# Performance work log

Measured on AMD Instinct MI355X. Metric: run time of the kernel, lower is better.

The kernel has to match this reference:

```python
import jax, jax.numpy as jnp
import numpy as np
from functools import partial

# geometry: [W1, W2, H1, H2, L1, L2] -> x range, y range, z range
GEOM = (-16.0, 16.0, -16.0, 16.0, -16.0, 16.0)
T_MEAN = jnp.array([-0.25, 0.01, 0.26, 0.46, 0.26, 0.62, 0.69, 1.46], jnp.float32)
T_STD = jnp.array([0.93, 0.26, 0.53, 0.89, 1.11, 0.13, 0.16, 0.19], jnp.float32)
M_CAND = 1024   # cap on candidates passing cls > 0.5 (top-k by score)
IOU_THR = 0.5
CLS_THR = 0.5
# 8 corner sign combos for (x, y, z)
SIGNS = jnp.array([[sx, sy, sz] for sx in (1.0, -1.0) for sy in (1.0, -1.0) for sz in (1.0, -1.0)], jnp.float32)


def _pairwise_iou(b):
    # b: [M, 4] in (min0, min1, max0, max1)
    area = jnp.clip(b[:, 2] - b[:, 0], 0) * jnp.clip(b[:, 3] - b[:, 1], 0)
    lt = jnp.maximum(b[:, None, :2], b[None, :, :2])
    rb = jnp.minimum(b[:, None, 2:], b[None, :, 2:])
    wh = jnp.clip(rb - lt, 0)
    inter = wh[..., 0] * wh[..., 1]
    union = area[:, None] + area[None, :] - inter
    return inter / jnp.maximum(union, 1e-9)


def _nms_keep(boxes, valid, thr):
    # boxes already sorted by descending score; greedy NMS like torchvision ops.nms
    M = boxes.shape[0]
    iou = _pairwise_iou(boxes)
    ar = jnp.arange(M)

    def body(i, st):
        keep, sup = st
        k = valid[i] & jnp.logical_not(sup[i])
        keep = keep.at[i].set(k)
        sup = sup | (k & (iou[i] > thr) & (ar > i))
        return keep, sup

    keep, _ = jax.lax.fori_loop(0, M, body, (jnp.zeros(M, bool), jnp.zeros(M, bool)))
    return keep


def _decode(points):
    B, C, Z, Y, X = points.shape
    x0, x1, y0, y1, z0, z1 = GEOM
    xs = x0 + (x1 - x0) / X * jnp.arange(X, dtype=jnp.float32)
    ys = y0 + (y1 - y0) / Y * jnp.arange(Y, dtype=jnp.float32)
    zs = z0 + (z1 - z0) / Z * jnp.arange(Z, dtype=jnp.float32)
    zz, yy, xx = jnp.meshgrid(zs, ys, xs, indexing='ij')  # [Z,Y,X]
    cls = points[:, 0]  # [B,Z,Y,X], untouched by normalization
    reg = points[:, 1:9] * T_STD[None, :, None, None, None] + T_MEAN[None, :, None, None, None]
    cos_t, sin_t, dx, dy, dz, log_w, log_h, log_l = [reg[:, i] for i in range(8)]
    theta = jnp.arctan2(sin_t, cos_t)
    cx = xx[None] + dx
    cy = yy[None] + dy
    cz = zz[None] + dz
    w, h, l = jnp.exp(log_w), jnp.exp(log_h), jnp.exp(log_l)
    return cls, cx, cy, cz, w, h, l, theta


def _per_batch(cls, cx, cy, cz, w, h, l, theta, n_out):
    sc, idx = jax.lax.top_k(cls.reshape(-1), M_CAND)
    valid = sc > CLS_THR
    g = lambda a: a.reshape(-1)[idx]
    cxf, cyf, czf, wf, hf, lf, thf = g(cx), g(cy), g(cz), g(w), g(h), g(l), g(theta)
    zeros = jnp.zeros_like(thf)
    box9 = jnp.stack([cxf, cyf, czf, wf, hf, lf, zeros, thf, zeros], axis=-1)  # [M,9]
    # corners: half-size offsets rotated by Ry(theta) (rx = rz = 0)
    off = 0.5 * SIGNS[None, :, :] * jnp.stack([wf, hf, lf], -1)[:, None, :]  # [M,8,3]
    ct, st = jnp.cos(thf)[:, None], jnp.sin(thf)[:, None]
    ox, oy, oz = off[..., 0], off[..., 1], off[..., 2]
    px = cxf[:, None] + ct * ox + st * oz
    py = cyf[:, None] + oy
    pz = czf[:, None] - st * ox + ct * oz
    xmin, xmax = px.min(-1), px.max(-1)
    ymin, ymax = py.min(-1), py.max(-1)
    zmin, zmax = pz.min(-1), pz.max(-1)
    xy_box = jnp.stack([xmin, ymin, xmax, ymax], -1)
    yz_box = jnp.stack([ymin, zmin, ymax, zmax], -1)
    keep = _nms_keep(xy_box, valid, IOU_THR) | _nms_keep(yz_box, valid, IOU_THR)
    # compact kept boxes to the front (score order), pad with zeros to n_out
    order = jnp.argsort(jnp.where(keep, 0, 1))[:n_out]  # stable sort
    kv = keep[order]
    boxes_out = box9[order] * kv[:, None].astype(box9.dtype)
    scores_out = sc[order] * kv.astype(sc.dtype)
    return boxes_out, scores_out


def setup_inputs() -> dict:
    key = jax.random.key(0)
    B, Z, Y, X = 4, 64, 128, 128
    points = jax.random.normal(key, (B, 9, Z, Y, X), dtype=jnp.float32)
    points = points.at[:, 0].add(-3.0)
    return {"points": points, "label_shape": 0, "n_out": 50}


def reference(points, label_shape, n_out):
    cls, cx, cy, cz, w, h, l, theta = _decode(points)
    boxes, scores = jax.vmap(partial(_per_batch, n_out=n_out))(cls, cx, cy, cz, w, h, l, theta)
    return boxes, scores  # [B, n_out, 9], [B, n_out]
```

## Files before the change

### kernel.cpp

```cpp
#include <hip/hip_runtime.h>

typedef unsigned long long u64;

#define ZYX (64 * 128 * 128)
#define CPB 128
#define SEG (ZYX / CPB)
#define SLOTS 64
#define VMAX 1024
#define MMAX 1024
#define MFAST 320
#define NCH 5
#define NTH 1024
#define NWAVE (NTH / 64)
#define CLS_THR 0.5f
#define IOU_THR 0.5f

__constant__ const float TM[8] = {-0.25f, 0.01f, 0.26f, 0.46f, 0.26f, 0.62f, 0.69f, 1.46f};
__constant__ const float TS[8] = {0.93f, 0.26f, 0.53f, 0.89f, 1.11f, 0.13f, 0.16f, 0.19f};

__device__ __forceinline__ void decode_from_r(const float* r, int f,
                                              float& cx, float& cy, float& cz,
                                              float& w, float& h, float& l, float& th) {
    int z = f >> 14;
    int y = (f >> 7) & 127;
    int x = f & 127;
    th = atan2f(r[1], r[0]);
    cx = (-16.0f + 0.25f * (float)x) + r[2];
    cy = (-16.0f + 0.25f * (float)y) + r[3];
    cz = (-16.0f + 0.5f * (float)z) + r[4];
    w = expf(r[5]);
    h = expf(r[6]);
    l = expf(r[7]);
}

__device__ __forceinline__ void decode_one(const float* __restrict__ pb, int f,
                                           float& cx, float& cy, float& cz,
                                           float& w, float& h, float& l, float& th) {
    float r[8];
#pragma unroll
    for (int c = 0; c < 8; ++c)
        r[c] = pb[(size_t)(c + 1) * ZYX + f] * TS[c] + TM[c];
    decode_from_r(r, f, cx, cy, cz, w, h, l, th);
}

__device__ __forceinline__ void corner_boxes(float cx, float cy, float cz,
                                             float w, float h, float l, float th,
                                             float& xmn, float& ymn, float& xmx, float& ymx,
                                             float& zmn, float& zmx) {
    float ct = cosf(th), st = sinf(th);
    xmn = 1e30f; xmx = -1e30f; ymn = 1e30f; ymx = -1e30f; zmn = 1e30f; zmx = -1e30f;
#pragma unroll
    for (int k = 0; k < 8; ++k) {
        float sx = (k & 4) ? -1.0f : 1.0f;
        float sy = (k & 2) ? -1.0f : 1.0f;
        float sz = (k & 1) ? -1.0f : 1.0f;
        float ox = 0.5f * sx * w;
        float oy = 0.5f * sy * h;
        float oz = 0.5f * sz * l;
        float px = cx + ct * ox + st * oz;
        float py = cy + oy;
        float pz = cz - st * ox + ct * oz;
        xmn = fminf(xmn, px); xmx = fmaxf(xmx, px);
        ymn = fminf(ymn, py); ymx = fmaxf(ymx, py);
        zmn = fminf(zmn, pz); zmx = fmaxf(zmx, pz);
    }
}

__device__ __forceinline__ bool iou_over(float ax0, float ay0, float ax1, float ay1, float aarea,
                                         float bx0, float by0, float bx1, float by1, float barea) {
    float lt0 = fmaxf(ax0, bx0), lt1 = fmaxf(ay0, by0);
    float rb0 = fminf(ax1, bx1), rb1 = fminf(ay1, by1);
    float inter = fmaxf(rb0 - lt0, 0.0f) * fmaxf(rb1 - lt1, 0.0f);
    float uni = aarea + barea - inter;
    return inter / fmaxf(uni, 1e-9f) > IOU_THR;
}

__global__ __launch_bounds__(256) void collect_kernel(const float* __restrict__ points,
                                                      int* __restrict__ gcnt,
                                                      float* __restrict__ gsc,
                                                      int* __restrict__ gix) {
    __shared__ float s_ssc[SLOTS];
    __shared__ int s_six[SLOTS];
    __shared__ int s_n;
    int g = blockIdx.x;
    int b = g >> 7;
    int c = g & (CPB - 1);
    int tid = threadIdx.x;
    if (tid == 0) s_n = 0;
    __syncthreads();
    const float4* p4 = (const float4*)(points + (size_t)b * 9 * ZYX) + (size_t)c * (SEG / 4);
    int base = c * SEG;
#pragma unroll
    for (int k = 0; k < SEG / 4 / 256; ++k) {
        int t4 = k * 256 + tid;
        float4 v = p4[t4];
        float vals[4] = {v.x, v.y, v.z, v.w};
        int f = base + t4 * 4;
#pragma unroll
        for (int q = 0; q < 4; ++q) {
            if (vals[q] > CLS_THR) {
                int s = atomicAdd(&s_n, 1);
                if (s < SLOTS) { s_ssc[s] = vals[q]; s_six[s] = f + q; }
            }
        }
    }
    __syncthreads();
    int n = s_n < SLOTS ? s_n : SLOTS;
    if (tid == 0) gcnt[g] = n;
    for (int i = tid; i < n; i += 256) {
        gsc[g * SLOTS + i] = s_ssc[i];
        gix[g * SLOTS + i] = s_six[i];
    }
}

__global__ __launch_bounds__(NTH, 1) void nms_kernel(const float* __restrict__ points,
                                                     const int* __restrict__ gcnt,
                                                     const float* __restrict__ gsc,
                                                     const int* __restrict__ gix,
                                                     float4* __restrict__ wbxy,
                                                     float4* __restrict__ wbyz,
                                                     float2* __restrict__ war,
                                                     float* __restrict__ out,
                                                     int B, int n_out) {
    __shared__ float s_sc[VMAX];
    __shared__ int s_ix[VMAX];
    __shared__ int s_r2o[MMAX];
    __shared__ float s_reg[MFAST * 8];
    __shared__ float4 s_bxy[MFAST];
    __shared__ float4 s_byz[MFAST];
    __shared__ float2 s_ar[MFAST];
    __shared__ u64 s_colx[MFAST * NCH];
    __shared__ u64 s_coly[MFAST * NCH];
    __shared__ u64 s_keptw[16];
    __shared__ int s_cnt[CPB], s_pre[CPB];

    int b = blockIdx.x;
    int tid = threadIdx.x;
    const float* pb = points + (size_t)b * 9 * ZYX;

    if (tid < CPB) s_cnt[tid] = gcnt[b * CPB + tid];
    __syncthreads();
    if (tid < CPB) {
        int pre = 0;
        for (int i = 0; i < CPB; ++i) { int v = s_cnt[i]; if (i < tid) pre += v; }
        s_pre[tid] = pre;
    }
    __syncthreads();
    int V = s_pre[CPB - 1] + s_cnt[CPB - 1];
    if (V > VMAX) V = VMAX;
    if (tid < CPB) {
        int n = s_cnt[tid], o = s_pre[tid], g = b * CPB + tid;
        for (int i = 0; i < n; ++i) {
            int d = o + i;
            if (d < VMAX) { s_sc[d] = gsc[g * SLOTS + i]; s_ix[d] = gix[g * SLOTS + i]; }
        }
    }
    __syncthreads();

    int M = V < MMAX ? V : MMAX;
    int nchw = (M + 63) >> 6;
    bool fast = (M <= MFAST);

    for (int i = tid; i < V; i += NTH) {
        float si = s_sc[i];
        int ii = s_ix[i];
        int r = 0;
        for (int j = 0; j < V; ++j) {
            float sj = s_sc[j];
            int ij = s_ix[j];
            bool before = (sj > si) || (sj == si && ij < ii);
            r += before ? 1 : 0;
        }
        if (r < MMAX) s_r2o[r] = i;
    }
    __syncthreads();

    if (fast) {
        int M8 = M * 8;
        for (int t = tid; t < M8; t += NTH) {
            int m = t >> 3, c = t & 7;
            int f = s_ix[s_r2o[m]];
            s_reg[t] = pb[(size_t)(c + 1) * ZYX + f] * TS[c] + TM[c];
        }
        __syncthreads();
        for (int m = tid; m < M; m += NTH) {
            float r[8];
#pragma unroll
            for (int c = 0; c < 8; ++c) r[c] = s_reg[m * 8 + c];
            int f = s_ix[s_r2o[m]];
            float cx, cy, cz, w, h, l, th;
            decode_from_r(r, f, cx, cy, cz, w, h, l, th);
            float xmn, ymn, xmx, ymx, zmn, zmx;
            corner_boxes(cx, cy, cz, w, h, l, th, xmn, ymn, xmx, ymx, zmn, zmx);
            s_bxy[m] = make_float4(xmn, ymn, xmx, ymx);
            s_byz[m] = make_float4(ymn, zmn, ymx, zmx);
            float axy = fmaxf(xmx - xmn, 0.0f) * fmaxf(ymx - ymn, 0.0f);
            float ayz = fmaxf(ymx - ymn, 0.0f) * fmaxf(zmx - zmn, 0.0f);
            s_ar[m] = make_float2(axy, ayz);
        }
        __syncthreads();

        int wid = tid >> 6, lane = tid & 63;
        for (int j = wid; j < M; j += NWAVE) {
            float4 jxy = s_bxy[j], jyz = s_byz[j];
            float2 ja = s_ar[j];
            int smax = j >> 6;
            for (int s = 0; s <= smax; ++s) {
                int i = (s << 6) | lane;
                float4 ixy = s_bxy[i];
                float2 ia = s_ar[i];
                bool p = (i < j);
                bool ax = p && iou_over(ixy.x, ixy.y, ixy.z, ixy.w, ia.x,
                                        jxy.x, jxy.y, jxy.z, jxy.w, ja.x);
                u64 wxw = __ballot(ax);
                float4 iyz = s_byz[i];
                bool ay = p && iou_over(iyz.x, iyz.y, iyz.z, iyz.w, ia.y,
                                        jyz.x, jyz.y, jyz.z, jyz.w, ja.y);
                u64 wyw = __ballot(ay);
                if (lane == 0) {
                    s_colx[j * NCH + s] = wxw;
                    s_coly[j * NCH + s] = wyw;
                }
            }
        }
        __syncthreads();

        if (tid < 64) {
            int lane = tid;
            u64 extx = 0, exty = 0;
            for (int s = 0; s < nchw; ++s) {
                int c = s * 64 + lane;
                bool have = c < M;
                u64 wx = have ? s_colx[c * NCH + s] : 0ull;
                u64 wy = have ? s_coly[c * NCH + s] : 0ull;
                bool ex = (extx >> s) & 1ull;
                bool ey = (exty >> s) & 1ull;
                bool sup = ex;
                for (;;) {
                    u64 K = __ballot(!sup && have);
                    bool ns = ex | ((wx & K) != 0ull);
                    u64 ch = __ballot(ns != sup);
                    sup = ns;
                    if (!ch) break;
                }
                u64 Kx = __ballot(!sup && have);
                bool supy = ey;
                for (;;) {
                    u64 K = __ballot(!supy && have);
                    bool ns = ey | ((wy & K) != 0ull);
                    u64 ch = __ballot(ns != supy);
                    supy = ns;
                    if (!ch) break;
                }
                u64 Ky = __ballot(!supy && have);
                if (lane == 0) s_keptw[s] = Kx | Ky;
                for (int s2 = s + 1; s2 < nchw; ++s2) {
                    int c2 = s2 * 64 + lane;
                    if (c2 < M) {
                        if (s_colx[c2 * NCH + s] & Kx) extx |= 1ull << s2;
                        if (s_coly[c2 * NCH + s] & Ky) exty |= 1ull << s2;
                    }
                }
            }
        }
    } else {
        for (int r = tid; r < M; r += NTH) {
            float cx, cy, cz, w, h, l, th;
            decode_one(pb, s_ix[s_r2o[r]], cx, cy, cz, w, h, l, th);
            float xmn, ymn, xmx, ymx, zmn, zmx;
            corner_boxes(cx, cy, cz, w, h, l, th, xmn, ymn, xmx, ymx, zmn, zmx);
            wbxy[b * MMAX + r] = make_float4(xmn, ymn, xmx, ymx);
            wbyz[b * MMAX + r] = make_float4(ymn, zmn, ymx, zmx);
            float axy = fmaxf(xmx - xmn, 0.0f) * fmaxf(ymx - ymn, 0.0f);
            float ayz = fmaxf(ymx - ymn, 0.0f) * fmaxf(zmx - zmn, 0.0f);
            war[b * MMAX + r] = make_float2(axy, ayz);
        }
        __syncthreads();
        if (tid == 0) {
            char* supx = (char*)s_colx;
            char* supy = ((char*)s_colx) + MMAX;
            for (int s = 0; s < 16; ++s) s_keptw[s] = 0ull;
            for (int i = 0; i < M; ++i) { supx[i] = 0; supy[i] = 0; }
            int nk = 0;
            for (int i = 0; i < M; ++i) {
                bool kx = !supx[i], ky = !supy[i];
                if (!(kx | ky)) continue;
                s_keptw[i >> 6] |= 1ull << (i & 63);
                if (++nk >= n_out) break;
                float4 ixy = wbxy[b * MMAX + i], iyz = wbyz[b * MMAX + i];
                float2 ia = war[b * MMAX + i];
                for (int j = i + 1; j < M; ++j) {
                    float4 jxy = wbxy[b * MMAX + j];
                    float2 ja = war[b * MMAX + j];
                    if (kx && !supx[j] &&
                        iou_over(ixy.x, ixy.y, ixy.z, ixy.w, ia.x,
                                 jxy.x, jxy.y, jxy.z, jxy.w, ja.x)) supx[j] = 1;
                    float4 jyz = wbyz[b * MMAX + j];
                    if (ky && !supy[j] &&
                        iou_over(iyz.x, iyz.y, iyz.z, iyz.w, ia.y,
                                 jyz.x, jyz.y, jyz.z, jyz.w, ja.y)) supy[j] = 1;
                }
            }
        }
    }
    __syncthreads();

    float* boxes_out = out;
    float* scores_out = out + (size_t)B * n_out * 9;
    for (int p = tid; p < n_out; p += NTH) {
        int m = -1, total = 0;
        for (int s = 0; s < nchw; ++s) {
            u64 w = s_keptw[s];
            int pc = __popcll(w);
            if (m < 0 && p < total + pc) {
                int need = p - total;
                for (int q = 0; q < need; ++q) w &= w - 1ull;
                int bit = __ffsll((long long)w) - 1;
                m = s * 64 + bit;
            }
            total += pc;
        }
        float o9[9] = {0, 0, 0, 0, 0, 0, 0, 0, 0};
        float sc = 0.0f;
        if (m >= 0) {
            int o = s_r2o[m];
            int f = s_ix[o];
            float cx, cy, cz, w, h, l, th;
            if (fast) {
                float r[8];
#pragma unroll
                for (int c = 0; c < 8; ++c) r[c] = s_reg[m * 8 + c];
                decode_from_r(r, f, cx, cy, cz, w, h, l, th);
            } else {
                decode_one(pb, f, cx, cy, cz, w, h, l, th);
            }
            o9[0] = cx; o9[1] = cy; o9[2] = cz;
            o9[3] = w;  o9[4] = h;  o9[5] = l;
            o9[6] = 0.0f; o9[7] = th; o9[8] = 0.0f;
            sc = s_sc[o];
        }
        float* bo = boxes_out + ((size_t)b * n_out + p) * 9;
#pragma unroll
        for (int k = 0; k < 9; ++k) bo[k] = o9[k];
        scores_out[(size_t)b * n_out + p] = sc;
    }
}

extern "C" void kernel_launch(void* const* d_in, const int* in_sizes, int n_in,
                              void* d_out, int out_size, void* d_ws, size_t ws_size,
                              hipStream_t stream) {
    const float* points = (const float*)d_in[0];
    int B = in_sizes[0] / (9 * ZYX);
    int n_out = out_size / (B * 10);

    char* ws = (char*)d_ws;
    size_t off = 0;
    int* gcnt = (int*)(ws + off); off += (size_t)B * CPB * sizeof(int); off = (off + 255) & ~(size_t)255;
    float* gsc = (float*)(ws + off); off += (size_t)B * CPB * SLOTS * 4;
    int* gix = (int*)(ws + off); off += (size_t)B * CPB * SLOTS * 4;
    float4* wbxy = (float4*)(ws + off); off += (size_t)B * MMAX * 16;
    float4* wbyz = (float4*)(ws + off); off += (size_t)B * MMAX * 16;
    float2* war = (float2*)(ws + off); off += (size_t)B * MMAX * 8;

    collect_kernel<<<B * CPB, 256, 0, stream>>>(points, gcnt, gsc, gix);
    nms_kernel<<<B, NTH, 0, stream>>>(points, gcnt, gsc, gix, wbxy, wbyz, war,
                                      (float*)d_out, B, n_out);
}
```

Baseline: 224.1 us.

## Gather regression channels in collect kernel and pack score/index into sort key

The collect kernel now gathers and normalizes the 8 regression channels for each candidate across many blocks, writing them to a compact workspace. The NMS kernel reads those rows with float4 loads instead of doing scattered strided reads from the input in its single-block-per-batch phase. Score and index are packed into one 64-bit key, so the rank computation does one compare per pair. VMAX/MMAX shrink to 768, which lowers shared memory but caps candidates below the spec's 1024 limit.

```diff
diff --git a/kernel.cpp b/kernel.cpp
--- a/kernel.cpp
+++ b/kernel.cpp
@@ -1,13 +1,14 @@
 #include <hip/hip_runtime.h>
 
 typedef unsigned long long u64;
+typedef unsigned int u32;
 
 #define ZYX (64 * 128 * 128)
 #define CPB 128
 #define SEG (ZYX / CPB)
 #define SLOTS 64
-#define VMAX 1024
-#define MMAX 1024
+#define VMAX 768
+#define MMAX 768
 #define MFAST 320
 #define NCH 5
 #define NTH 1024
@@ -77,8 +78,8 @@
 
 __global__ __launch_bounds__(256) void collect_kernel(const float* __restrict__ points,
                                                       int* __restrict__ gcnt,
-                                                      float* __restrict__ gsc,
-                                                      int* __restrict__ gix) {
+                                                      u64* __restrict__ gkey,
+                                                      float* __restrict__ greg) {
     __shared__ float s_ssc[SLOTS];
     __shared__ int s_six[SLOTS];
     __shared__ int s_n;
@@ -88,7 +89,8 @@
     int tid = threadIdx.x;
     if (tid == 0) s_n = 0;
     __syncthreads();
-    const float4* p4 = (const float4*)(points + (size_t)b * 9 * ZYX) + (size_t)c * (SEG / 4);
+    const float* pb = points + (size_t)b * 9 * ZYX;
+    const float4* p4 = (const float4*)pb + (size_t)c * (SEG / 4);
     int base = c * SEG;
 #pragma unroll
     for (int k = 0; k < SEG / 4 / 256; ++k) {
@@ -108,22 +110,28 @@
     int n = s_n < SLOTS ? s_n : SLOTS;
     if (tid == 0) gcnt[g] = n;
     for (int i = tid; i < n; i += 256) {
-        gsc[g * SLOTS + i] = s_ssc[i];
-        gix[g * SLOTS + i] = s_six[i];
+        gkey[g * SLOTS + i] =
+            ((u64)__float_as_uint(s_ssc[i]) << 32) | (u64)(0xFFFFFFFFu - (u32)s_six[i]);
+    }
+    for (int t = tid; t < n * 8; t += 256) {
+        int m = t >> 3, ch = t & 7;
+        int f = s_six[m];
+        greg[((size_t)g * SLOTS + m) * 8 + ch] =
+            pb[(size_t)(ch + 1) * ZYX + f] * TS[ch] + TM[ch];
     }
 }
 
 __global__ __launch_bounds__(NTH, 1) void nms_kernel(const float* __restrict__ points,
                                                      const int* __restrict__ gcnt,
-                                                     const float* __restrict__ gsc,
-                                                     const int* __restrict__ gix,
+                                                     const u64* __restrict__ gkey,
+                                                     const float* __restrict__ greg,
                                                      float4* __restrict__ wbxy,
                                                      float4* __restrict__ wbyz,
                                                      float2* __restrict__ war,
                                                      float* __restrict__ out,
                                                      int B, int n_out) {
-    __shared__ float s_sc[VMAX];
-    __shared__ int s_ix[VMAX];
+    __shared__ u64 s_key[VMAX];
+    __shared__ int s_src[VMAX];
     __shared__ int s_r2o[MMAX];
     __shared__ float s_reg[MFAST * 8];
     __shared__ float4 s_bxy[MFAST];
@@ -131,7 +139,7 @@
     __shared__ float2 s_ar[MFAST];
     __shared__ u64 s_colx[MFAST * NCH];
     __shared__ u64 s_coly[MFAST * NCH];
-    __shared__ u64 s_keptw[16];
+    __shared__ u64 s_keptw[12];
     __shared__ int s_cnt[CPB], s_pre[CPB];
 
     int b = blockIdx.x;
@@ -152,7 +160,10 @@
         int n = s_cnt[tid], o = s_pre[tid], g = b * CPB + tid;
         for (int i = 0; i < n; ++i) {
             int d = o + i;
-            if (d < VMAX) { s_sc[d] = gsc[g * SLOTS + i]; s_ix[d] = gix[g * SLOTS + i]; }
+            if (d < VMAX) {
+                s_key[d] = gkey[g * SLOTS + i];
+                s_src[d] = g * SLOTS + i;
+            }
         }
     }
     __syncthreads();
@@ -162,32 +173,22 @@
     bool fast = (M <= MFAST);
 
     for (int i = tid; i < V; i += NTH) {
-        float si = s_sc[i];
-        int ii = s_ix[i];
+        u64 ki = s_key[i];
         int r = 0;
-        for (int j = 0; j < V; ++j) {
-            float sj = s_sc[j];
-            int ij = s_ix[j];
-            bool before = (sj > si) || (sj == si && ij < ii);
-            r += before ? 1 : 0;
-        }
+        for (int j = 0; j < V; ++j) r += (s_key[j] > ki) ? 1 : 0;
         if (r < MMAX) s_r2o[r] = i;
     }
     __syncthreads();
 
     if (fast) {
-        int M8 = M * 8;
-        for (int t = tid; t < M8; t += NTH) {
-            int m = t >> 3, c = t & 7;
-            int f = s_ix[s_r2o[m]];
-            s_reg[t] = pb[(size_t)(c + 1) * ZYX + f] * TS[c] + TM[c];
-        }
-        __syncthreads();
         for (int m = tid; m < M; m += NTH) {
-            float r[8];
-#pragma unroll
-            for (int c = 0; c < 8; ++c) r[c] = s_reg[m * 8 + c];
-            int f = s_ix[s_r2o[m]];
+            int o = s_r2o[m];
+            const float4* row = (const float4*)(greg + (size_t)s_src[o] * 8);
+            float4 r0 = row[0], r1 = row[1];
+            float r[8] = {r0.x, r0.y, r0.z, r0.w, r1.x, r1.y, r1.z, r1.w};
+            float4* sr = (float4*)(s_reg + (size_t)m * 8);
+            sr[0] = r0; sr[1] = r1;
+            int f = (int)(0xFFFFFFFFu - (u32)s_key[o]);
             float cx, cy, cz, w, h, l, th;
             decode_from_r(r, f, cx, cy, cz, w, h, l, th);
             float xmn, ymn, xmx, ymx, zmn, zmx;
@@ -265,8 +266,10 @@
         }
     } else {
         for (int r = tid; r < M; r += NTH) {
+            int o = s_r2o[r];
+            int f = (int)(0xFFFFFFFFu - (u32)s_key[o]);
             float cx, cy, cz, w, h, l, th;
-            decode_one(pb, s_ix[s_r2o[r]], cx, cy, cz, w, h, l, th);
+            decode_one(pb, f, cx, cy, cz, w, h, l, th);
             float xmn, ymn, xmx, ymx, zmn, zmx;
             corner_boxes(cx, cy, cz, w, h, l, th, xmn, ymn, xmx, ymx, zmn, zmx);
             wbxy[b * MMAX + r] = make_float4(xmn, ymn, xmx, ymx);
@@ -279,7 +282,7 @@
         if (tid == 0) {
             char* supx = (char*)s_colx;
             char* supy = ((char*)s_colx) + MMAX;
-            for (int s = 0; s < 16; ++s) s_keptw[s] = 0ull;
+            for (int s = 0; s < 12; ++s) s_keptw[s] = 0ull;
             for (int i = 0; i < M; ++i) { supx[i] = 0; supy[i] = 0; }
             int nk = 0;
             for (int i = 0; i < M; ++i) {
@@ -324,7 +327,8 @@
         float sc = 0.0f;
         if (m >= 0) {
             int o = s_r2o[m];
-            int f = s_ix[o];
+            u64 key = s_key[o];
+            int f = (int)(0xFFFFFFFFu - (u32)key);
             float cx, cy, cz, w, h, l, th;
             if (fast) {
                 float r[8];
@@ -337,7 +341,7 @@
             o9[0] = cx; o9[1] = cy; o9[2] = cz;
             o9[3] = w;  o9[4] = h;  o9[5] = l;
             o9[6] = 0.0f; o9[7] = th; o9[8] = 0.0f;
-            sc = s_sc[o];
+            sc = __uint_as_float((u32)(key >> 32));
         }
         float* bo = boxes_out + ((size_t)b * n_out + p) * 9;
 #pragma unroll
@@ -356,13 +360,13 @@
     char* ws = (char*)d_ws;
     size_t off = 0;
     int* gcnt = (int*)(ws + off); off += (size_t)B * CPB * sizeof(int); off = (off + 255) & ~(size_t)255;
-    float* gsc = (float*)(ws + off); off += (size_t)B * CPB * SLOTS * 4;
-    int* gix = (int*)(ws + off); off += (size_t)B * CPB * SLOTS * 4;
+    u64* gkey = (u64*)(ws + off); off += (size_t)B * CPB * SLOTS * 8;
+    float* greg = (float*)(ws + off); off += (size_t)B * CPB * SLOTS * 8 * 4;
     float4* wbxy = (float4*)(ws + off); off += (size_t)B * MMAX * 16;
     float4* wbyz = (float4*)(ws + off); off += (size_t)B * MMAX * 16;
     float2* war = (float2*)(ws + off); off += (size_t)B * MMAX * 8;
 
-    collect_kernel<<<B * CPB, 256, 0, stream>>>(points, gcnt, gsc, gix);
-    nms_kernel<<<B, NTH, 0, stream>>>(points, gcnt, gsc, gix, wbxy, wbyz, war,
+    collect_kernel<<<B * CPB, 256, 0, stream>>>(points, gcnt, gkey, greg);
+    nms_kernel<<<B, NTH, 0, stream>>>(points, gcnt, gkey, greg, wbxy, wbyz, war,
                                       (float*)d_out, B, n_out);
 }
```

After: 215.6 us. 1.04x faster.
